# Kernel optimization log

Hardware: AMD Instinct MI355X
Metric: run time of the kernel (lower is better)

Reference implementation:

```python
import math
import jax, jax.numpy as jnp
import numpy as np

L = 16
LOG2T = 19
T = 1 << LOG2T
F = 2
N_MIN = 16
N_MAX = 2048
N_PTS = 1048576

# intended geometric growth factor (source has a parenthesization bug)
_B = math.exp((math.log(N_MAX) - math.log(N_MIN)) / (L - 1))
RESOLUTIONS = [int(math.floor(N_MIN * (_B ** i))) for i in range(L)]

# 8 corner offsets of a voxel, [8, 3]
_OFFS_NP = np.stack(np.meshgrid([0, 1], [0, 1], [0, 1], indexing='ij'), -1).reshape(8, 3)
# spatial hash primes from Instant-NGP
_PRIMES_NP = np.array([1, 2654435761, 805459861], dtype=np.uint32)


def setup_inputs() -> dict:
    key = jax.random.key(0)
    k1, k2 = jax.random.split(key)
    x = jax.random.uniform(k1, (N_PTS, 3), dtype=jnp.float32)  # positions in [0,1)
    table = jax.random.normal(k2, (L, T, F), dtype=jnp.float32) * 1e-4
    return {"x": x, "table": table}


def _encode(x, table):
    offs_i = jnp.asarray(_OFFS_NP, dtype=jnp.uint32)          # [8,3]
    offs_f = jnp.asarray(_OFFS_NP, dtype=x.dtype)             # [8,3]
    primes = jnp.asarray(_PRIMES_NP)                          # [3] uint32
    mask = jnp.uint32(T - 1)
    outs = []
    for lvl in range(L):
        res = RESOLUTIONS[lvl]
        xs = x * res                                           # [N,3]
        x0 = jnp.floor(xs)
        w = xs - x0                                            # [N,3] trilerp weights
        # corner integer coords, [N,8,3]
        c = x0.astype(jnp.uint32)[:, None, :] + offs_i[None]
        # spatial hash: xor of coord*prime, masked to T (T is a power of 2)
        hp = c * primes                                        # uint32 wraparound mul
        h = (hp[..., 0] ^ hp[..., 1] ^ hp[..., 2]) & mask      # [N,8]
        feats = table[lvl][h.astype(jnp.int32)]                # [N,8,F] gather
        # trilinear weights: prod over dims of (w if corner==1 else 1-w)
        wts = jnp.prod(jnp.where(offs_f[None] == 1.0, w[:, None, :], 1.0 - w[:, None, :]), axis=-1)  # [N,8]
        outs.append(jnp.einsum('nc,ncf->nf', wts, feats))      # [N,F]
    return jnp.concatenate(outs, axis=-1)                      # [N, L*F]


def reference(x, table):
    return _encode(x, table)
```

## Files before the change

### kernel.cpp

```cpp
#include <hip/hip_runtime.h>
#include <cmath>

#define NPTS   1048576
#define NLVL   16
#define T      (1u << 19)
#define TMASK  (T - 1u)
#define P1     2654435761u
#define P2     805459861u

typedef float    v2f __attribute__((ext_vector_type(2)));
typedef float    v4f __attribute__((ext_vector_type(4)));
typedef _Float16 v2h __attribute__((ext_vector_type(2)));
typedef _Float16 v4h __attribute__((ext_vector_type(4)));

struct Corners { uint32_t h[8]; float wt[8]; };
struct RfArr   { float r[NLVL]; };

__device__ __forceinline__ Corners mk_corners(float px, float py, float pz, float rf) {
    Corners cc;
    const float xs0 = px * rf, xs1 = py * rf, xs2 = pz * rf;
    const float f0 = floorf(xs0), f1 = floorf(xs1), f2 = floorf(xs2);
    const float w0 = xs0 - f0, w1 = xs1 - f1, w2 = xs2 - f2;
    const uint32_t i0 = (uint32_t)f0, i1 = (uint32_t)f1, i2 = (uint32_t)f2;
    const uint32_t A0 = i0,      A1 = i0 + 1u;
    const uint32_t B0 = i1 * P1, B1 = B0 + P1;
    const uint32_t C0 = i2 * P2, C1 = C0 + P2;
    cc.h[0] = (A0 ^ B0 ^ C0) & TMASK;  cc.h[1] = (A0 ^ B0 ^ C1) & TMASK;
    cc.h[2] = (A0 ^ B1 ^ C0) & TMASK;  cc.h[3] = (A0 ^ B1 ^ C1) & TMASK;
    cc.h[4] = (A1 ^ B0 ^ C0) & TMASK;  cc.h[5] = (A1 ^ B0 ^ C1) & TMASK;
    cc.h[6] = (A1 ^ B1 ^ C0) & TMASK;  cc.h[7] = (A1 ^ B1 ^ C1) & TMASK;
    const float u0 = 1.0f - w0, u1 = 1.0f - w1, u2 = 1.0f - w2;
    cc.wt[0] = (u0 * u1) * u2;  cc.wt[1] = (u0 * u1) * w2;
    cc.wt[2] = (u0 * w1) * u2;  cc.wt[3] = (u0 * w1) * w2;
    cc.wt[4] = (w0 * u1) * u2;  cc.wt[5] = (w0 * u1) * w2;
    cc.wt[6] = (w0 * w1) * u2;  cc.wt[7] = (w0 * w1) * w2;
    return cc;
}

__global__ __launch_bounds__(256) void hashgrid_mega(
    const float* __restrict__ x,
    const float* __restrict__ table,
    _Float16* __restrict__ ws,
    RfArr rfa)
{
    const int   lvl = blockIdx.y;
    const float rf  = rfa.r[lvl];
    const float* __restrict__ tb  = table + ((size_t)lvl << 20);
    _Float16*  __restrict__   wsl = ws    + ((size_t)lvl << 21);

    const int t = blockIdx.x * 256 + threadIdx.x;

    const v2f q0 = __builtin_nontemporal_load((const v2f*)(x + 6 * (size_t)t + 0));
    const v2f q1 = __builtin_nontemporal_load((const v2f*)(x + 6 * (size_t)t + 2));
    const v2f q2 = __builtin_nontemporal_load((const v2f*)(x + 6 * (size_t)t + 4));

    const Corners c0 = mk_corners(q0.x, q0.y, q1.x, rf);
    const Corners c1 = mk_corners(q1.y, q2.x, q2.y, rf);

    float a00 = 0.f, a01 = 0.f, a10 = 0.f, a11 = 0.f;
#pragma unroll
    for (int c = 0; c < 8; ++c) {
        const float2 g0 = *(const float2*)(tb + 2 * (size_t)c0.h[c]);
        const float2 g1 = *(const float2*)(tb + 2 * (size_t)c1.h[c]);
        a00 += c0.wt[c] * g0.x;  a01 += c0.wt[c] * g0.y;
        a10 += c1.wt[c] * g1.x;  a11 += c1.wt[c] * g1.y;
    }
    v4h r;
    r.x = (_Float16)a00;  r.y = (_Float16)a01;
    r.z = (_Float16)a10;  r.w = (_Float16)a11;
    __builtin_nontemporal_store(r, (v4h*)(wsl + 4 * (size_t)t));
}

__global__ __launch_bounds__(256) void hashgrid_transpose2(
    const _Float16* __restrict__ ws,
    float* __restrict__ out)
{
    const int t = blockIdx.x * 256 + threadIdx.x;
    float acc0[2 * NLVL], acc1[2 * NLVL];
#pragma unroll
    for (int l = 0; l < NLVL; ++l) {
        const v4h g = __builtin_nontemporal_load(
            (const v4h*)(ws + ((size_t)l << 21) + 4 * (size_t)t));
        acc0[2 * l + 0] = (float)g.x;
        acc0[2 * l + 1] = (float)g.y;
        acc1[2 * l + 0] = (float)g.z;
        acc1[2 * l + 1] = (float)g.w;
    }
    v4f* o0 = (v4f*)(out + (size_t)(2 * t) * 32);
    v4f* o1 = (v4f*)(out + (size_t)(2 * t + 1) * 32);
#pragma unroll
    for (int k = 0; k < 8; ++k) {
        v4f v0; v0.x = acc0[4*k]; v0.y = acc0[4*k+1]; v0.z = acc0[4*k+2]; v0.w = acc0[4*k+3];
        o0[k] = v0;
    }
#pragma unroll
    for (int k = 0; k < 8; ++k) {
        v4f v1; v1.x = acc1[4*k]; v1.y = acc1[4*k+1]; v1.z = acc1[4*k+2]; v1.w = acc1[4*k+3];
        o1[k] = v1;
    }
}

__global__ __launch_bounds__(256) void hashgrid_lvl_direct(
    const float* __restrict__ x,
    const float* __restrict__ tb,
    float* __restrict__ outl,
    float rf)
{
    const int n = blockIdx.x * 256 + threadIdx.x;
    const float px = __builtin_nontemporal_load(x + 3 * (size_t)n + 0);
    const float py = __builtin_nontemporal_load(x + 3 * (size_t)n + 1);
    const float pz = __builtin_nontemporal_load(x + 3 * (size_t)n + 2);
    const Corners cc = mk_corners(px, py, pz, rf);
    float a0 = 0.f, a1 = 0.f;
#pragma unroll
    for (int c = 0; c < 8; ++c) {
        const float2 g = *(const float2*)(tb + 2 * (size_t)cc.h[c]);
        a0 += cc.wt[c] * g.x;
        a1 += cc.wt[c] * g.y;
    }
    outl[(size_t)n * 32 + 0] = a0;
    outl[(size_t)n * 32 + 1] = a1;
}

extern "C" void kernel_launch(void* const* d_in, const int* in_sizes, int n_in,
                              void* d_out, int out_size, void* d_ws, size_t ws_size,
                              hipStream_t stream) {
    const float* x     = (const float*)d_in[0];
    const float* table = (const float*)d_in[1];
    float* out         = (float*)d_out;
    _Float16* ws       = (_Float16*)d_ws;

    double (*volatile p_log)(double)          = log;
    double (*volatile p_exp)(double)          = exp;
    double (*volatile p_pow)(double, double)  = pow;
    double (*volatile p_floor)(double)        = floor;

    const double b = p_exp((p_log(2048.0) - p_log(16.0)) / 15.0);
    RfArr rfa;
    for (int l = 0; l < NLVL; ++l)
        rfa.r[l] = (float)(int)p_floor(16.0 * p_pow(b, (double)l));

    const bool use_ws = ws_size >= (size_t)NLVL * NPTS * 2 * sizeof(_Float16);

    if (!use_ws) {
        for (int l = 0; l < NLVL; ++l)
            hashgrid_lvl_direct<<<NPTS / 256, 256, 0, stream>>>(
                x, table + ((size_t)l << 20), out + 2 * l, rfa.r[l]);
        return;
    }

    dim3 grid(NPTS / 512, NLVL);
    hashgrid_mega<<<grid, 256, 0, stream>>>(x, table, ws, rfa);
    hashgrid_transpose2<<<NPTS / 512, 256, 0, stream>>>(ws, out);
}
```

Measured before the change: 612.3 us.

## Split coarse levels into fused multi-level kernel, launch fine levels sequentially

The five coarsest levels, whose tables are small enough to stay cache-resident, are now handled by one kernel that loops over them per point and reuses the loaded position. The remaining fine levels get one launch each instead of a single 2D grid, so each launch touches only one level's table at a time, which is meant to improve L2 locality for the gathers. This adds eleven extra kernel launches and serializes the fine levels, and the coarse-level kernel does more work per thread.

Result: faster. 572.2 us (-6.5%).

```diff
diff --git a/kernel.cpp b/kernel.cpp
--- a/kernel.cpp
+++ b/kernel.cpp
@@ -3,6 +3,7 @@
 
 #define NPTS   1048576
 #define NLVL   16
+#define NLOW   5
 #define T      (1u << 19)
 #define TMASK  (T - 1u)
 #define P1     2654435761u
@@ -37,17 +38,12 @@
     return cc;
 }
 
-__global__ __launch_bounds__(256) void hashgrid_mega(
+__global__ __launch_bounds__(256) void hashgrid_lvl2pt(
     const float* __restrict__ x,
-    const float* __restrict__ table,
-    _Float16* __restrict__ ws,
-    RfArr rfa)
+    const float* __restrict__ tb,
+    _Float16* __restrict__ wsl,
+    float rf)
 {
-    const int   lvl = blockIdx.y;
-    const float rf  = rfa.r[lvl];
-    const float* __restrict__ tb  = table + ((size_t)lvl << 20);
-    _Float16*  __restrict__   wsl = ws    + ((size_t)lvl << 21);
-
     const int t = blockIdx.x * 256 + threadIdx.x;
 
     const v2f q0 = __builtin_nontemporal_load((const v2f*)(x + 6 * (size_t)t + 0));
@@ -69,6 +65,34 @@
     r.x = (_Float16)a00;  r.y = (_Float16)a01;
     r.z = (_Float16)a10;  r.w = (_Float16)a11;
     __builtin_nontemporal_store(r, (v4h*)(wsl + 4 * (size_t)t));
+}
+
+__global__ __launch_bounds__(256) void hashgrid_low(
+    const float* __restrict__ x,
+    const float* __restrict__ table,
+    _Float16* __restrict__ ws,
+    float r0, float r1, float r2, float r3, float r4)
+{
+    const int n = blockIdx.x * 256 + threadIdx.x;
+    const float px = __builtin_nontemporal_load(x + 3 * (size_t)n + 0);
+    const float py = __builtin_nontemporal_load(x + 3 * (size_t)n + 1);
+    const float pz = __builtin_nontemporal_load(x + 3 * (size_t)n + 2);
+
+    const float rs[NLOW] = {r0, r1, r2, r3, r4};
+#pragma unroll
+    for (int l = 0; l < NLOW; ++l) {
+        const Corners cc = mk_corners(px, py, pz, rs[l]);
+        const float* tb = table + ((size_t)l << 20);
+        float a0 = 0.f, a1 = 0.f;
+#pragma unroll
+        for (int c = 0; c < 8; ++c) {
+            const float2 g = *(const float2*)(tb + 2 * (size_t)cc.h[c]);
+            a0 += cc.wt[c] * g.x;
+            a1 += cc.wt[c] * g.y;
+        }
+        v2h r; r.x = (_Float16)a0; r.y = (_Float16)a1;
+        __builtin_nontemporal_store(r, (v2h*)(ws + ((size_t)l << 21) + 2 * (size_t)n));
+    }
 }
 
 __global__ __launch_bounds__(256) void hashgrid_transpose2(
@@ -149,7 +173,11 @@
         return;
     }
 
-    dim3 grid(NPTS / 512, NLVL);
-    hashgrid_mega<<<grid, 256, 0, stream>>>(x, table, ws, rfa);
+    for (int l = NLOW; l < NLVL; ++l) {
+        hashgrid_lvl2pt<<<NPTS / 512, 256, 0, stream>>>(
+            x, table + ((size_t)l << 20), ws + ((size_t)l << 21), rfa.r[l]);
+    }
+    hashgrid_low<<<NPTS / 256, 256, 0, stream>>>(
+        x, table, ws, rfa.r[0], rfa.r[1], rfa.r[2], rfa.r[3], rfa.r[4]);
     hashgrid_transpose2<<<NPTS / 512, 256, 0, stream>>>(ws, out);
 }
```

## Pair x-adjacent corner gathers into one 16-byte load and split level launches

Applied to the files above, without the earlier changes.

The x-neighbour corners hash to A0 and A0+1 with the same B/C terms. When i0 is even, that pair occupies adjacent table entries, so a single aligned float4 load returns both corners. When i0 is odd, a second float2 load is issued instead. This is meant to cut the number of gather transactions per point by up to half. It also replaces the single 2D-grid launch with one launch per high level (5..15) plus one combined launch for levels 0-4, likely so each launch keeps one level's table resident in cache. The extra launches add overhead, and the branch on i0 parity diverges within a wave.

After: 550.2 us. 10.1% less time.

```diff
diff --git a/kernel.cpp b/kernel.cpp
--- a/kernel.cpp
+++ b/kernel.cpp
@@ -3,6 +3,7 @@
 
 #define NPTS   1048576
 #define NLVL   16
+#define NLOW   5
 #define T      (1u << 19)
 #define TMASK  (T - 1u)
 #define P1     2654435761u
@@ -13,11 +14,12 @@
 typedef _Float16 v2h __attribute__((ext_vector_type(2)));
 typedef _Float16 v4h __attribute__((ext_vector_type(4)));
 
-struct Corners { uint32_t h[8]; float wt[8]; };
-struct RfArr   { float r[NLVL]; };
+struct RfArr { float r[NLVL]; };
 
-__device__ __forceinline__ Corners mk_corners(float px, float py, float pz, float rf) {
-    Corners cc;
+__device__ __forceinline__ void encode_pt(
+    const float* __restrict__ tb, float px, float py, float pz, float rf,
+    float& ra0, float& ra1)
+{
     const float xs0 = px * rf, xs1 = py * rf, xs2 = pz * rf;
     const float f0 = floorf(xs0), f1 = floorf(xs1), f2 = floorf(xs2);
     const float w0 = xs0 - f0, w1 = xs1 - f1, w2 = xs2 - f2;
@@ -25,25 +27,44 @@
     const uint32_t A0 = i0,      A1 = i0 + 1u;
     const uint32_t B0 = i1 * P1, B1 = B0 + P1;
     const uint32_t C0 = i2 * P2, C1 = C0 + P2;
-    cc.h[0] = (A0 ^ B0 ^ C0) & TMASK;  cc.h[1] = (A0 ^ B0 ^ C1) & TMASK;
-    cc.h[2] = (A0 ^ B1 ^ C0) & TMASK;  cc.h[3] = (A0 ^ B1 ^ C1) & TMASK;
-    cc.h[4] = (A1 ^ B0 ^ C0) & TMASK;  cc.h[5] = (A1 ^ B0 ^ C1) & TMASK;
-    cc.h[6] = (A1 ^ B1 ^ C0) & TMASK;  cc.h[7] = (A1 ^ B1 ^ C1) & TMASK;
+    const bool odd = (i0 & 1u) != 0u;
     const float u0 = 1.0f - w0, u1 = 1.0f - w1, u2 = 1.0f - w2;
-    cc.wt[0] = (u0 * u1) * u2;  cc.wt[1] = (u0 * u1) * w2;
-    cc.wt[2] = (u0 * w1) * u2;  cc.wt[3] = (u0 * w1) * w2;
-    cc.wt[4] = (w0 * u1) * u2;  cc.wt[5] = (w0 * u1) * w2;
-    cc.wt[6] = (w0 * w1) * u2;  cc.wt[7] = (w0 * w1) * w2;
-    return cc;
+    const float wb[2] = {u1, w1};
+    const float wc[2] = {u2, w2};
+
+    float a0 = 0.f, a1 = 0.f;
+#pragma unroll
+    for (int b = 0; b < 2; ++b) {
+#pragma unroll
+        for (int c = 0; c < 2; ++c) {
+            const uint32_t hBC = (b ? B1 : B0) ^ (c ? C1 : C0);
+            const uint32_t h0  = (A0 ^ hBC) & TMASK;
+            const uint32_t e   = h0 & ~1u;
+            const v4f gq = *(const v4f*)(tb + 2 * (size_t)e);
+            const bool hi = (h0 & 1u) != 0u;
+            v2f g0, g1;
+            g0.x = hi ? gq.z : gq.x;   g0.y = hi ? gq.w : gq.y;
+            g1.x = hi ? gq.x : gq.z;   g1.y = hi ? gq.y : gq.w;
+            if (odd) {
+                const uint32_t h1 = (A1 ^ hBC) & TMASK;
+                g1 = *(const v2f*)(tb + 2 * (size_t)h1);
+            }
+            const float wt0 = (u0 * wb[b]) * wc[c];
+            const float wt1 = (w0 * wb[b]) * wc[c];
+            a0 += wt0 * g0.x;  a1 += wt0 * g0.y;
+            a0 += wt1 * g1.x;  a1 += wt1 * g1.y;
+        }
+    }
+    ra0 = a0; ra1 = a1;
 }
 
-__global__ __launch_bounds__(256) void hashgrid_mega(
+__global__ __launch_bounds__(256) void hashgrid_lvl(
     const float* __restrict__ x,
     const float* __restrict__ table,
     _Float16* __restrict__ ws,
-    RfArr rfa)
+    RfArr rfa, int lvl_base)
 {
-    const int   lvl = blockIdx.y;
+    const int   lvl = lvl_base + blockIdx.y;
     const float rf  = rfa.r[lvl];
     const float* __restrict__ tb  = table + ((size_t)lvl << 20);
     _Float16*  __restrict__   wsl = ws    + ((size_t)lvl << 21);
@@ -54,17 +75,10 @@
     const v2f q1 = __builtin_nontemporal_load((const v2f*)(x + 6 * (size_t)t + 2));
     const v2f q2 = __builtin_nontemporal_load((const v2f*)(x + 6 * (size_t)t + 4));
 
-    const Corners c0 = mk_corners(q0.x, q0.y, q1.x, rf);
-    const Corners c1 = mk_corners(q1.y, q2.x, q2.y, rf);
+    float a00, a01, a10, a11;
+    encode_pt(tb, q0.x, q0.y, q1.x, rf, a00, a01);
+    encode_pt(tb, q1.y, q2.x, q2.y, rf, a10, a11);
 
-    float a00 = 0.f, a01 = 0.f, a10 = 0.f, a11 = 0.f;
-#pragma unroll
-    for (int c = 0; c < 8; ++c) {
-        const float2 g0 = *(const float2*)(tb + 2 * (size_t)c0.h[c]);
-        const float2 g1 = *(const float2*)(tb + 2 * (size_t)c1.h[c]);
-        a00 += c0.wt[c] * g0.x;  a01 += c0.wt[c] * g0.y;
-        a10 += c1.wt[c] * g1.x;  a11 += c1.wt[c] * g1.y;
-    }
     v4h r;
     r.x = (_Float16)a00;  r.y = (_Float16)a01;
     r.z = (_Float16)a10;  r.w = (_Float16)a11;
@@ -110,14 +124,8 @@
     const float px = __builtin_nontemporal_load(x + 3 * (size_t)n + 0);
     const float py = __builtin_nontemporal_load(x + 3 * (size_t)n + 1);
     const float pz = __builtin_nontemporal_load(x + 3 * (size_t)n + 2);
-    const Corners cc = mk_corners(px, py, pz, rf);
-    float a0 = 0.f, a1 = 0.f;
-#pragma unroll
-    for (int c = 0; c < 8; ++c) {
-        const float2 g = *(const float2*)(tb + 2 * (size_t)cc.h[c]);
-        a0 += cc.wt[c] * g.x;
-        a1 += cc.wt[c] * g.y;
-    }
+    float a0, a1;
+    encode_pt(tb, px, py, pz, rf, a0, a1);
     outl[(size_t)n * 32 + 0] = a0;
     outl[(size_t)n * 32 + 1] = a1;
 }
@@ -149,7 +157,13 @@
         return;
     }
 
-    dim3 grid(NPTS / 512, NLVL);
-    hashgrid_mega<<<grid, 256, 0, stream>>>(x, table, ws, rfa);
+    for (int l = NLOW; l < NLVL; ++l) {
+        dim3 g(NPTS / 512, 1);
+        hashgrid_lvl<<<g, 256, 0, stream>>>(x, table, ws, rfa, l);
+    }
+    {
+        dim3 g(NPTS / 512, NLOW);
+        hashgrid_lvl<<<g, 256, 0, stream>>>(x, table, ws, rfa, 0);
+    }
     hashgrid_transpose2<<<NPTS / 512, 256, 0, stream>>>(ws, out);
 }
```
